# Performance work log

Hardware: AMD Instinct MI355X
Metric: run time of the kernel (lower is better)

The kernel has to match this reference:

```python
import jax, jax.numpy as jnp
import numpy as np

B, T, D, H, E, K = 2, 1024, 1024, 16, 8, 2
HS = D // H
FF = 4 * D


def layernorm(x, g, b, eps=1e-5):
    m = jnp.mean(x, axis=-1, keepdims=True)
    v = jnp.mean((x - m) ** 2, axis=-1, keepdims=True)
    return (x - m) * jax.lax.rsqrt(v + eps) * g + b


def setup_inputs() -> dict:
    key = jax.random.key(0)
    ks = jax.random.split(key, 10)
    s = 0.02
    return {
        "x": jax.random.normal(ks[0], (B, T, D), jnp.float32),
        "Wq": jax.random.normal(ks[1], (H, D, HS), jnp.float32) * s,
        "Wk": jax.random.normal(ks[2], (H, D, HS), jnp.float32) * s,
        "Wv": jax.random.normal(ks[3], (H, D, HS), jnp.float32) * s,
        "gate_W": jax.random.normal(ks[4], (D, E), jnp.float32) * s,
        "W1": jax.random.normal(ks[5], (E, D, FF), jnp.float32) * s,
        "b1": jnp.zeros((E, FF), jnp.float32),
        "W2": jax.random.normal(ks[6], (E, FF, D), jnp.float32) * s,
        "b2": jnp.zeros((E, D), jnp.float32),
        "ln1_g": jnp.ones((D,), jnp.float32),
        "ln1_b": jnp.zeros((D,), jnp.float32),
        "ln2_g": jnp.ones((D,), jnp.float32),
        "ln2_b": jnp.zeros((D,), jnp.float32),
    }


def reference(x, Wq, Wk, Wv, gate_W, W1, b1, W2, b2, ln1_g, ln1_b, ln2_g, ln2_b):
    b, t, d = x.shape
    # --- multi-head causal attention (note: original scales by n_embed**-0.5) ---
    q = jnp.einsum("btd,hdf->bhtf", x, Wq)
    k = jnp.einsum("btd,hdf->bhtf", x, Wk)
    v = jnp.einsum("btd,hdf->bhtf", x, Wv)
    wei = jnp.einsum("bhtf,bhsf->bhts", q, k) * (d ** -0.5)
    mask = jnp.tril(jnp.ones((t, t), bool))
    wei = jnp.where(mask, wei, -jnp.inf)
    wei = jax.nn.softmax(wei, axis=-1)
    attn = jnp.einsum("bhts,bhsf->bhtf", wei, v)
    attn = attn.transpose(0, 2, 1, 3).reshape(b, t, d)  # concat heads

    y = x + layernorm(attn, ln1_g, ln1_b)

    # --- MoE: top-k gate, softmax over selected logits, weighted combine ---
    flat = y.reshape(-1, d)                         # [N, D]
    logits = flat @ gate_W                          # [N, E]
    topv, topi = jax.lax.top_k(logits, K)           # [N, K]
    w = jax.nn.softmax(topv, axis=-1)               # [N, K]
    combine = jnp.sum(jax.nn.one_hot(topi, E, dtype=flat.dtype) * w[..., None], axis=1)  # [N, E]

    h = jax.nn.relu(jnp.einsum("nd,edf->enf", flat, W1) + b1[:, None, :])  # [E, N, FF]
    eo = jnp.einsum("enf,efd->end", h, W2) + b2[:, None, :]                # [E, N, D]
    moe = jnp.einsum("ne,end->nd", combine, eo)                            # [N, D]

    out = y + layernorm(moe.reshape(b, t, d), ln2_g, ln2_b)
    return out
```

## Files before the change

### kernel.cpp

```cpp
#include <hip/hip_runtime.h>
#include <hip/hip_bf16.h>
#include <math.h>

typedef short short8 __attribute__((ext_vector_type(8)));
typedef float floatx4 __attribute__((ext_vector_type(4)));
typedef unsigned int u32_g __attribute__((address_space(1)));
typedef unsigned int u32_l __attribute__((address_space(3)));

__device__ __forceinline__ void gl_lds16(const void* g, void* l) {
    __builtin_amdgcn_global_load_lds((const u32_g*)g, (u32_l*)l, 16, 0, 0);
}

#define NB 2
#define TSEQ 1024
#define DIM 1024
#define NHEAD 16
#define HS 64
#define NEXP 8
#define FF 4096
#define NTOK (NB*TSEQ)
#define MAXSLOT 5120

#define OFF_Q      ((size_t)0)
#define OFF_K      ((size_t)8388608)
#define OFF_V      ((size_t)16777216)
#define OFF_ATTN   ((size_t)25165824)
#define OFF_Y      ((size_t)33554432)
#define OFF_YBF    ((size_t)41943040)
#define OFF_W1T    ((size_t)46137344)
#define OFF_MOE    ((size_t)113246208)
#define OFF_TOPKE  ((size_t)121634816)
#define OFF_TOPKW  ((size_t)121651200)
#define OFF_CNT    ((size_t)121667584)
#define OFF_PO     ((size_t)121667648)
#define OFF_CUR    ((size_t)121667712)
#define OFF_SLOTT  ((size_t)121667776)
#define OFF_SLOTW  ((size_t)121688256)
#define OFF_S      ((size_t)121708800)
#define OFF_XHI    (OFF_S)
#define OFF_XLO    (OFF_S + 4194304)
#define OFF_WTHI   (OFF_S + 8388608)
#define OFF_WTLO   (OFF_S + 14680064)
#define OFF_W2T    (OFF_S)
#define OFF_H      (OFF_S + 67108864)

__global__ __launch_bounds__(256) void xsplit_kernel(
    const float* __restrict__ x, __hip_bfloat16* __restrict__ xhi, __hip_bfloat16* __restrict__ xlo)
{
    int idx = (blockIdx.x * 256 + threadIdx.x) * 4;
    float4 v = *(const float4*)(x + idx);
    float vv[4] = {v.x, v.y, v.z, v.w};
    union { ushort u[4]; ushort4 q; } hi, lo;
    #pragma unroll
    for (int l = 0; l < 4; ++l) {
        __hip_bfloat16 hb = __float2bfloat16(vv[l]);
        hi.u[l] = *(const ushort*)&hb;
        float r = vv[l] - __bfloat162float(hb);
        __hip_bfloat16 lb = __float2bfloat16(r);
        lo.u[l] = *(const ushort*)&lb;
    }
    *(ushort4*)((ushort*)xhi + idx) = hi.q;
    *(ushort4*)((ushort*)xlo + idx) = lo.q;
}

__global__ __launch_bounds__(256) void wsplit_kernel(
    const float* __restrict__ Wq, const float* __restrict__ Wk, const float* __restrict__ Wv,
    __hip_bfloat16* __restrict__ Wthi, __hip_bfloat16* __restrict__ Wtlo)
{
    int z = blockIdx.z, mat = z >> 4, hh = z & 15;
    const float* W = (mat == 0) ? Wq : ((mat == 1) ? Wk : Wv);
    const float* slab = W + (size_t)hh * DIM * HS;
    ushort* ohi = (ushort*)Wthi + (size_t)mat * (DIM * DIM) + (size_t)hh * HS * DIM;
    ushort* olo = (ushort*)Wtlo + (size_t)mat * (DIM * DIM) + (size_t)hh * HS * DIM;
    int c0 = blockIdx.x * 32, r0 = blockIdx.y * 32;
    __shared__ float tile[32][33];
    int t = threadIdx.x, i = t >> 3, j4 = (t & 7) * 4;
    float4 v4 = *(const float4*)(slab + (size_t)(r0 + i) * HS + c0 + j4);
    tile[i][j4] = v4.x; tile[i][j4+1] = v4.y; tile[i][j4+2] = v4.z; tile[i][j4+3] = v4.w;
    __syncthreads();
    union { ushort u[4]; ushort4 q; } hi, lo;
    #pragma unroll
    for (int l = 0; l < 4; ++l) {
        float xv = tile[j4 + l][i];
        __hip_bfloat16 hb = __float2bfloat16(xv);
        hi.u[l] = *(const ushort*)&hb;
        float r = xv - __bfloat162float(hb);
        __hip_bfloat16 lb = __float2bfloat16(r);
        lo.u[l] = *(const ushort*)&lb;
    }
    *(ushort4*)(ohi + (size_t)(c0 + i) * DIM + r0 + j4) = hi.q;
    *(ushort4*)(olo + (size_t)(c0 + i) * DIM + r0 + j4) = lo.q;
}

__global__ __launch_bounds__(256) void qkv_mfma(
    const __hip_bfloat16* __restrict__ xhi, const __hip_bfloat16* __restrict__ xlo,
    const __hip_bfloat16* __restrict__ Wthi, const __hip_bfloat16* __restrict__ Wtlo,
    float* __restrict__ Q, float* __restrict__ Kb, float* __restrict__ V)
{
    int mat = blockIdx.z;
    const __hip_bfloat16* Bhg = Wthi + (size_t)mat * (DIM * DIM);
    const __hip_bfloat16* Blg = Wtlo + (size_t)mat * (DIM * DIM);
    float* O = (mat == 0) ? Q : ((mat == 1) ? Kb : V);
    int n0 = blockIdx.x * 64, m0 = blockIdx.y * 128;
    int t = threadIdx.x, wave = t >> 6, lane = t & 63;
    __shared__ __hip_bfloat16 Ah[128][32];
    __shared__ __hip_bfloat16 Al[128][32];
    __shared__ __hip_bfloat16 Bh[64][32];
    __shared__ __hip_bfloat16 Bl[64][32];
    const __hip_bfloat16 *gAh[2], *gAl[2];
    __hip_bfloat16 *lAh[2], *lAl[2];
    #pragma unroll
    for (int p = 0; p < 2; ++p) {
        int lin = p * 256 + t, row = lin >> 2, seg = lin & 3;
        gAh[p] = xhi + (size_t)(m0 + row) * DIM + seg * 8;
        gAl[p] = xlo + (size_t)(m0 + row) * DIM + seg * 8;
        int cb = p * 256 + wave * 64;
        lAh[p] = &Ah[0][0] + (size_t)cb * 8;
        lAl[p] = &Al[0][0] + (size_t)cb * 8;
    }
    const __hip_bfloat16* gBh = Bhg + (size_t)(n0 + (t >> 2)) * DIM + (t & 3) * 8;
    const __hip_bfloat16* gBl = Blg + (size_t)(n0 + (t >> 2)) * DIM + (t & 3) * 8;
    __hip_bfloat16* lBh = &Bh[0][0] + (size_t)(wave * 64) * 8;
    __hip_bfloat16* lBl = &Bl[0][0] + (size_t)(wave * 64) * 8;

    int wr = (wave >> 1) * 64, wcl = (wave & 1) * 32;
    int lrow = lane & 15, quad = lane >> 4;
    floatx4 acc[4][2];
    #pragma unroll
    for (int i = 0; i < 4; ++i)
        #pragma unroll
        for (int j = 0; j < 2; ++j) acc[i][j] = (floatx4){0.f, 0.f, 0.f, 0.f};

    for (int k0 = 0; k0 < DIM; k0 += 32) {
        __syncthreads();
        gl_lds16(gAh[0] + k0, lAh[0]); gl_lds16(gAh[1] + k0, lAh[1]);
        gl_lds16(gAl[0] + k0, lAl[0]); gl_lds16(gAl[1] + k0, lAl[1]);
        gl_lds16(gBh + k0, lBh);       gl_lds16(gBl + k0, lBl);
        __syncthreads();
        short8 ah[4], al[4], bh[2], bl[2];
        #pragma unroll
        for (int i = 0; i < 4; ++i) {
            ah[i] = *(const short8*)(&Ah[wr + i * 16 + lrow][quad * 8]);
            al[i] = *(const short8*)(&Al[wr + i * 16 + lrow][quad * 8]);
        }
        #pragma unroll
        for (int j = 0; j < 2; ++j) {
            bh[j] = *(const short8*)(&Bh[wcl + j * 16 + lrow][quad * 8]);
            bl[j] = *(const short8*)(&Bl[wcl + j * 16 + lrow][quad * 8]);
        }
        #pragma unroll
        for (int i = 0; i < 4; ++i)
            #pragma unroll
            for (int j = 0; j < 2; ++j) {
                acc[i][j] = __builtin_amdgcn_mfma_f32_16x16x32_bf16(ah[i], bh[j], acc[i][j], 0, 0, 0);
                acc[i][j] = __builtin_amdgcn_mfma_f32_16x16x32_bf16(ah[i], bl[j], acc[i][j], 0, 0, 0);
                acc[i][j] = __builtin_amdgcn_mfma_f32_16x16x32_bf16(al[i], bh[j], acc[i][j], 0, 0, 0);
            }
    }
    #pragma unroll
    for (int i = 0; i < 4; ++i)
        #pragma unroll
        for (int j = 0; j < 2; ++j) {
            int ng = n0 + wcl + j * 16 + lrow;
            int hh = ng >> 6, f = ng & 63;
            #pragma unroll
            for (int r = 0; r < 4; ++r) {
                int mg = m0 + wr + i * 16 + quad * 4 + r;
                int bb = mg >> 10, tt = mg & 1023;
                O[(((size_t)bb * NHEAD + hh) * TSEQ + tt) * HS + f] = acc[i][j][r];
            }
        }
}

__global__ __launch_bounds__(256) void scores_kernel(
    const float* __restrict__ Q, const float* __restrict__ Kb, float* __restrict__ S)
{
    int tri = blockIdx.x, bh = blockIdx.y;
    int mt = 0; while (((mt + 1) * (mt + 2)) / 2 <= tri) ++mt;
    int nt = tri - (mt * (mt + 1)) / 2;
    int m0 = mt * 128, n0 = nt * 128;
    const float* Qb = Q + (size_t)bh * TSEQ * HS;
    const float* Kh = Kb + (size_t)bh * TSEQ * HS;
    float* Sb = S + (size_t)bh * TSEQ * TSEQ;
    __shared__ float As[16][132];
    __shared__ float Bs[16][132];
    int t = threadIdx.x, tx = t & 15, ty = t >> 4;
    float acc[8][8] = {{0.f}};
    for (int k0 = 0; k0 < HS; k0 += 16) {
        #pragma unroll
        for (int pss = 0; pss < 2; ++pss) {
            int lin = pss * 256 + t, m = lin >> 2, c = lin & 3;
            float4 v4 = *(const float4*)(Qb + (size_t)(m0 + m) * HS + k0 + c * 4);
            As[c*4+0][m] = v4.x; As[c*4+1][m] = v4.y; As[c*4+2][m] = v4.z; As[c*4+3][m] = v4.w;
        }
        #pragma unroll
        for (int pss = 0; pss < 2; ++pss) {
            int lin = pss * 256 + t, s = lin >> 2, c = lin & 3;
            float4 v4 = *(const float4*)(Kh + (size_t)(n0 + s) * HS + k0 + c * 4);
            Bs[c*4+0][s] = v4.x; Bs[c*4+1][s] = v4.y; Bs[c*4+2][s] = v4.z; Bs[c*4+3][s] = v4.w;
        }
        __syncthreads();
        #pragma unroll
        for (int kk = 0; kk < 16; ++kk) {
            float a[8], b[8];
            *(float4*)a       = *(const float4*)(&As[kk][ty * 4]);
            *(float4*)(a + 4) = *(const float4*)(&As[kk][64 + ty * 4]);
            *(float4*)b       = *(const float4*)(&Bs[kk][tx * 4]);
            *(float4*)(b + 4) = *(const float4*)(&Bs[kk][64 + tx * 4]);
            #pragma unroll
            for (int i = 0; i < 8; ++i)
                #pragma unroll
                for (int j = 0; j < 8; ++j) acc[i][j] += a[i] * b[j];
        }
        __syncthreads();
    }
    const float scale = 0.03125f;
    #pragma unroll
    for (int i = 0; i < 8; ++i) {
        int r = m0 + ((i < 4) ? ty * 4 + i : 64 + ty * 4 + (i - 4));
        #pragma unroll
        for (int jg = 0; jg < 2; ++jg) {
            int cb = n0 + ((jg == 0) ? tx * 4 : 64 + tx * 4);
            float4 v4 = make_float4(acc[i][jg*4+0]*scale, acc[i][jg*4+1]*scale,
                                    acc[i][jg*4+2]*scale, acc[i][jg*4+3]*scale);
            *(float4*)(Sb + (size_t)r * TSEQ + cb) = v4;
        }
    }
}

__global__ __launch_bounds__(256) void softmax_kernel(float* __restrict__ S)
{
    int row = blockIdx.x, bh = row >> 10, r = row & 1023;
    float* p = S + ((size_t)bh * TSEQ + r) * TSEQ;
    int len = r + 1, t = threadIdx.x;
    float v[4]; float mx = -1e30f;
    #pragma unroll
    for (int i = 0; i < 4; ++i) { int c = t + i * 256; v[i] = (c < len) ? p[c] : -1e30f; mx = fmaxf(mx, v[i]); }
    __shared__ float redA[4];
    #pragma unroll
    for (int off = 32; off; off >>= 1) mx = fmaxf(mx, __shfl_down(mx, off));
    if ((t & 63) == 0) redA[t >> 6] = mx;
    __syncthreads();
    mx = fmaxf(fmaxf(redA[0], redA[1]), fmaxf(redA[2], redA[3]));
    float sum = 0.f;
    #pragma unroll
    for (int i = 0; i < 4; ++i) { int c = t + i * 256; float e = (c < len) ? expf(v[i] - mx) : 0.f; v[i] = e; sum += e; }
    __shared__ float redB[4];
    #pragma unroll
    for (int off = 32; off; off >>= 1) sum += __shfl_down(sum, off);
    if ((t & 63) == 0) redB[t >> 6] = sum;
    __syncthreads();
    float inv = 1.f / (redB[0] + redB[1] + redB[2] + redB[3]);
    #pragma unroll
    for (int i = 0; i < 4; ++i) { int c = t + i * 256; p[c] = v[i] * inv; }
}

__global__ __launch_bounds__(256) void pv_kernel(
    const float* __restrict__ S, const float* __restrict__ V, float* __restrict__ attn)
{
    int mt = blockIdx.x, bh = blockIdx.y;
    int m0 = mt * 128;
    const float* P = S + (size_t)bh * TSEQ * TSEQ;
    const float* Vb = V + (size_t)bh * TSEQ * HS;
    __shared__ float As[16][132];
    __shared__ float Bs[16][68];
    int t = threadIdx.x, tx = t & 15, ty = t >> 4;
    float acc[8][4] = {{0.f}};
    int kend = m0 + 128;
    for (int k0 = 0; k0 < kend; k0 += 16) {
        #pragma unroll
        for (int pss = 0; pss < 2; ++pss) {
            int lin = pss * 256 + t, m = lin >> 2, c = lin & 3;
            float4 v4 = *(const float4*)(P + (size_t)(m0 + m) * TSEQ + k0 + c * 4);
            As[c*4+0][m] = v4.x; As[c*4+1][m] = v4.y; As[c*4+2][m] = v4.z; As[c*4+3][m] = v4.w;
        }
        { int kk = t >> 4, c = t & 15;
          float4 v4 = *(const float4*)(Vb + (size_t)(k0 + kk) * HS + c * 4);
          *(float4*)(&Bs[kk][c * 4]) = v4; }
        __syncthreads();
        #pragma unroll
        for (int kk = 0; kk < 16; ++kk) {
            float a[8], b[4];
            *(float4*)a       = *(const float4*)(&As[kk][ty * 4]);
            *(float4*)(a + 4) = *(const float4*)(&As[kk][64 + ty * 4]);
            *(float4*)b       = *(const float4*)(&Bs[kk][tx * 4]);
            #pragma unroll
            for (int i = 0; i < 8; ++i)
                #pragma unroll
                for (int j = 0; j < 4; ++j) acc[i][j] += a[i] * b[j];
        }
        __syncthreads();
    }
    int b = bh >> 4, hh = bh & 15;
    #pragma unroll
    for (int i = 0; i < 8; ++i) {
        int r = m0 + ((i < 4) ? ty * 4 + i : 64 + ty * 4 + (i - 4));
        float4 v4 = make_float4(acc[i][0], acc[i][1], acc[i][2], acc[i][3]);
        *(float4*)(attn + ((size_t)b * TSEQ + r) * DIM + hh * HS + tx * 4) = v4;
    }
}

__global__ __launch_bounds__(256) void ln1_kernel(
    const float* __restrict__ x, const float* __restrict__ attn,
    const float* __restrict__ g, const float* __restrict__ bta,
    float* __restrict__ y, __hip_bfloat16* __restrict__ ybf)
{
    int n = blockIdx.x, t = threadIdx.x;
    const float* a = attn + (size_t)n * DIM;
    float v[4]; float s = 0.f;
    #pragma unroll
    for (int i = 0; i < 4; ++i) { v[i] = a[t + i * 256]; s += v[i]; }
    __shared__ float redA[4];
    #pragma unroll
    for (int off = 32; off; off >>= 1) s += __shfl_down(s, off);
    if ((t & 63) == 0) redA[t >> 6] = s;
    __syncthreads();
    float mean = (redA[0] + redA[1] + redA[2] + redA[3]) * (1.f / 1024.f);
    float s2 = 0.f;
    #pragma unroll
    for (int i = 0; i < 4; ++i) { float d = v[i] - mean; s2 += d * d; }
    __shared__ float redB[4];
    #pragma unroll
    for (int off = 32; off; off >>= 1) s2 += __shfl_down(s2, off);
    if ((t & 63) == 0) redB[t >> 6] = s2;
    __syncthreads();
    float rstd = rsqrtf((redB[0] + redB[1] + redB[2] + redB[3]) * (1.f / 1024.f) + 1e-5f);
    #pragma unroll
    for (int i = 0; i < 4; ++i) {
        int d = t + i * 256;
        float val = x[(size_t)n * DIM + d] + (v[i] - mean) * rstd * g[d] + bta[d];
        y[(size_t)n * DIM + d] = val;
        ybf[(size_t)n * DIM + d] = __float2bfloat16(val);
    }
}

__global__ __launch_bounds__(256) void transpose_kernel(
    const float* __restrict__ in, __hip_bfloat16* __restrict__ out, int R, int C)
{
    const float* ie = in + (size_t)blockIdx.z * R * C;
    __hip_bfloat16* oe = out + (size_t)blockIdx.z * R * C;
    int c0 = blockIdx.x * 32, r0 = blockIdx.y * 32;
    __shared__ float tile[32][33];
    int t = threadIdx.x, i = t >> 3, j4 = (t & 7) * 4;
    float4 v4 = *(const float4*)(ie + (size_t)(r0 + i) * C + c0 + j4);
    tile[i][j4] = v4.x; tile[i][j4+1] = v4.y; tile[i][j4+2] = v4.z; tile[i][j4+3] = v4.w;
    __syncthreads();
    union { ushort u[4]; ushort4 v; } pk;
    #pragma unroll
    for (int l = 0; l < 4; ++l) {
        __hip_bfloat16 hb = __float2bfloat16(tile[j4 + l][i]);
        pk.u[l] = *(const ushort*)&hb;
    }
    *(ushort4*)((ushort*)oe + (size_t)(c0 + i) * R + r0 + j4) = pk.v;
}

__global__ __launch_bounds__(256) void gate_kernel(
    const float* __restrict__ y, const float* __restrict__ gW,
    int* __restrict__ topk_e, float* __restrict__ topk_w, int* __restrict__ cnt)
{
    int n = blockIdx.x, t = threadIdx.x;
    const float* yr = y + (size_t)n * DIM;
    float p[8] = {0.f,0.f,0.f,0.f,0.f,0.f,0.f,0.f};
    for (int d = t; d < DIM; d += 256) {
        float yv = yr[d];
        const float* w = gW + (size_t)d * NEXP;
        #pragma unroll
        for (int e = 0; e < 8; ++e) p[e] += yv * w[e];
    }
    #pragma unroll
    for (int e = 0; e < 8; ++e)
        #pragma unroll
        for (int off = 32; off; off >>= 1) p[e] += __shfl_down(p[e], off);
    __shared__ float lg[4][8];
    if ((t & 63) == 0) { int w = t >> 6;
        #pragma unroll
        for (int e = 0; e < 8; ++e) lg[w][e] = p[e]; }
    __syncthreads();
    if (t == 0) {
        float l[8];
        #pragma unroll
        for (int e = 0; e < 8; ++e) l[e] = lg[0][e] + lg[1][e] + lg[2][e] + lg[3][e];
        int e0 = 0; float v0 = l[0];
        for (int e = 1; e < 8; ++e) if (l[e] > v0) { v0 = l[e]; e0 = e; }
        int e1 = 0; float v1 = -1e30f;
        for (int e = 0; e < 8; ++e) if (e != e0 && l[e] > v1) { v1 = l[e]; e1 = e; }
        float z = expf(v1 - v0);
        float w0 = 1.f / (1.f + z), w1 = z / (1.f + z);
        topk_e[n * 2] = e0; topk_e[n * 2 + 1] = e1;
        topk_w[n * 2] = w0; topk_w[n * 2 + 1] = w1;
        atomicAdd(&cnt[e0], 1); atomicAdd(&cnt[e1], 1);
    }
}

__global__ void scan_kernel(const int* __restrict__ cnt, int* __restrict__ po, int* __restrict__ cursor)
{
    if (threadIdx.x == 0 && blockIdx.x == 0) {
        int acc = 0;
        for (int e = 0; e < 8; ++e) { po[e] = acc; cursor[e] = acc; acc += ((cnt[e] + 127) >> 7) << 7; }
        po[8] = acc;
    }
}

__global__ void scatter_kernel(const int* __restrict__ topk_e, const float* __restrict__ topk_w,
                               int* __restrict__ cursor, int* __restrict__ slot_token, float* __restrict__ slot_w)
{
    int i = blockIdx.x * 256 + threadIdx.x;
    int e = topk_e[i];
    int pos = atomicAdd(&cursor[e], 1);
    slot_token[pos] = i >> 1;
    slot_w[pos] = topk_w[i];
}

__global__ __launch_bounds__(256) void moe_gemm1(
    const __hip_bfloat16* __restrict__ ybf, const __hip_bfloat16* __restrict__ W1t,
    const float* __restrict__ b1, const int* __restrict__ po, const int* __restrict__ cnt,
    const int* __restrict__ slot_token, __hip_bfloat16* __restrict__ h)
{
    int m0 = blockIdx.y * 128;
    int total = po[8];
    if (m0 >= total) return;
    int e = 0;
    for (int i = 0; i < 8; ++i) if (m0 >= po[i] && m0 < po[i + 1]) e = i;
    int valid = po[e] + cnt[e] - m0; if (valid > 128) valid = 128;
    int n0 = blockIdx.x * 128;
    int t = threadIdx.x, wave = t >> 6, lane = t & 63;
    __shared__ int tok[128];
    __shared__ __hip_bfloat16 As[128][64];
    __shared__ __hip_bfloat16 Bs[128][64];
    if (t < 128) tok[t] = (t < valid) ? slot_token[m0 + t] : slot_token[m0];
    __syncthreads();
    const __hip_bfloat16 *gA[4], *gB[4];
    __hip_bfloat16 *lA[4], *lB[4];
    #pragma unroll
    for (int p = 0; p < 4; ++p) {
        int lin = p * 256 + t, row = lin >> 3, seg = lin & 7;
        gA[p] = ybf + (size_t)tok[row] * DIM + seg * 8;
        gB[p] = W1t + ((size_t)e * FF + n0 + row) * DIM + seg * 8;
        int cb = p * 256 + wave * 64;
        lA[p] = &As[0][0] + (size_t)cb * 8;
        lB[p] = &Bs[0][0] + (size_t)cb * 8;
    }
    int wr = (wave >> 1) * 64, wc = (wave & 1) * 64;
    int lrow = lane & 15, quad = lane >> 4;
    floatx4 acc[4][4];
    #pragma unroll
    for (int i = 0; i < 4; ++i)
        #pragma unroll
        for (int j = 0; j < 4; ++j) acc[i][j] = (floatx4){0.f, 0.f, 0.f, 0.f};
    for (int k0 = 0; k0 < DIM; k0 += 64) {
        __syncthreads();
        #pragma unroll
        for (int p = 0; p < 4; ++p) { gl_lds16(gA[p] + k0, lA[p]); gl_lds16(gB[p] + k0, lB[p]); }
        __syncthreads();
        #pragma unroll
        for (int ks = 0; ks < 2; ++ks) {
            short8 a[4], b[4];
            #pragma unroll
            for (int i = 0; i < 4; ++i) a[i] = *(const short8*)(&As[wr + i * 16 + lrow][ks * 32 + quad * 8]);
            #pragma unroll
            for (int j = 0; j < 4; ++j) b[j] = *(const short8*)(&Bs[wc + j * 16 + lrow][ks * 32 + quad * 8]);
            #pragma unroll
            for (int i = 0; i < 4; ++i)
                #pragma unroll
                for (int j = 0; j < 4; ++j)
                    acc[i][j] = __builtin_amdgcn_mfma_f32_16x16x32_bf16(a[i], b[j], acc[i][j], 0, 0, 0);
        }
    }
    #pragma unroll
    for (int i = 0; i < 4; ++i)
        #pragma unroll
        for (int j = 0; j < 4; ++j) {
            int col = n0 + wc + j * 16 + lrow;
            float bias = b1[e * FF + col];
            #pragma unroll
            for (int r = 0; r < 4; ++r) {
                int row = wr + i * 16 + quad * 4 + r;
                float vv = fmaxf(acc[i][j][r] + bias, 0.f);
                h[(size_t)(m0 + row) * FF + col] = __float2bfloat16(vv);
            }
        }
}

__global__ __launch_bounds__(256) void moe_gemm2(
    const __hip_bfloat16* __restrict__ h, const __hip_bfloat16* __restrict__ W2t,
    const float* __restrict__ b2, const int* __restrict__ po, const int* __restrict__ cnt,
    const int* __restrict__ slot_token, const float* __restrict__ slot_w, float* __restrict__ moe)
{
    int m0 = blockIdx.y * 128;
    int total = po[8];
    if (m0 >= total) return;
    int e = 0;
    for (int i = 0; i < 8; ++i) if (m0 >= po[i] && m0 < po[i + 1]) e = i;
    int valid = po[e] + cnt[e] - m0; if (valid > 128) valid = 128;
    int n0 = blockIdx.x * 128;
    int kz = blockIdx.z;
    int t = threadIdx.x, wave = t >> 6, lane = t & 63;
    __shared__ int tokS[128];
    __shared__ float wS[128];
    __shared__ __hip_bfloat16 As[128][64];
    __shared__ __hip_bfloat16 Bs[128][64];
    if (t < 128) {
        tokS[t] = (t < valid) ? slot_token[m0 + t] : 0;
        wS[t]   = (t < valid) ? slot_w[m0 + t] : 0.f;
    }
    __syncthreads();
    const __hip_bfloat16 *gA[4], *gB[4];
    __hip_bfloat16 *lA[4], *lB[4];
    #pragma unroll
    for (int p = 0; p < 4; ++p) {
        int lin = p * 256 + t, row = lin >> 3, seg = lin & 7;
        gA[p] = h + (size_t)(m0 + row) * FF + seg * 8;
        gB[p] = W2t + ((size_t)e * DIM + n0 + row) * FF + seg * 8;
        int cb = p * 256 + wave * 64;
        lA[p] = &As[0][0] + (size_t)cb * 8;
        lB[p] = &Bs[0][0] + (size_t)cb * 8;
    }
    int wr = (wave >> 1) * 64, wc = (wave & 1) * 64;
    int lrow = lane & 15, quad = lane >> 4;
    floatx4 acc[4][4];
    #pragma unroll
    for (int i = 0; i < 4; ++i)
        #pragma unroll
        for (int j = 0; j < 4; ++j) acc[i][j] = (floatx4){0.f, 0.f, 0.f, 0.f};
    int kbeg = kz * (FF / 2), kend = kbeg + (FF / 2);
    for (int k0 = kbeg; k0 < kend; k0 += 64) {
        __syncthreads();
        #pragma unroll
        for (int p = 0; p < 4; ++p) { gl_lds16(gA[p] + k0, lA[p]); gl_lds16(gB[p] + k0, lB[p]); }
        __syncthreads();
        #pragma unroll
        for (int ks = 0; ks < 2; ++ks) {
            short8 a[4], b[4];
            #pragma unroll
            for (int i = 0; i < 4; ++i) a[i] = *(const short8*)(&As[wr + i * 16 + lrow][ks * 32 + quad * 8]);
            #pragma unroll
            for (int j = 0; j < 4; ++j) b[j] = *(const short8*)(&Bs[wc + j * 16 + lrow][ks * 32 + quad * 8]);
            #pragma unroll
            for (int i = 0; i < 4; ++i)
                #pragma unroll
                for (int j = 0; j < 4; ++j)
                    acc[i][j] = __builtin_amdgcn_mfma_f32_16x16x32_bf16(a[i], b[j], acc[i][j], 0, 0, 0);
        }
    }
    #pragma unroll
    for (int i = 0; i < 4; ++i)
        #pragma unroll
        for (int j = 0; j < 4; ++j) {
            int col = n0 + wc + j * 16 + lrow;
            float bias = (kz == 0) ? b2[e * DIM + col] : 0.f;
            #pragma unroll
            for (int r = 0; r < 4; ++r) {
                int row = wr + i * 16 + quad * 4 + r;
                if (row < valid) {
                    float vv = acc[i][j][r] + bias;
                    atomicAdd(&moe[(size_t)tokS[row] * DIM + col], wS[row] * vv);
                }
            }
        }
}

__global__ __launch_bounds__(256) void ln2_kernel(
    const float* __restrict__ y, const float* __restrict__ moe,
    const float* __restrict__ g, const float* __restrict__ bta, float* __restrict__ out)
{
    int n = blockIdx.x, t = threadIdx.x;
    const float* a = moe + (size_t)n * DIM;
    float v[4]; float s = 0.f;
    #pragma unroll
    for (int i = 0; i < 4; ++i) { v[i] = a[t + i * 256]; s += v[i]; }
    __shared__ float redA[4];
    #pragma unroll
    for (int off = 32; off; off >>= 1) s += __shfl_down(s, off);
    if ((t & 63) == 0) redA[t >> 6] = s;
    __syncthreads();
    float mean = (redA[0] + redA[1] + redA[2] + redA[3]) * (1.f / 1024.f);
    float s2 = 0.f;
    #pragma unroll
    for (int i = 0; i < 4; ++i) { float d = v[i] - mean; s2 += d * d; }
    __shared__ float redB[4];
    #pragma unroll
    for (int off = 32; off; off >>= 1) s2 += __shfl_down(s2, off);
    if ((t & 63) == 0) redB[t >> 6] = s2;
    __syncthreads();
    float rstd = rsqrtf((redB[0] + redB[1] + redB[2] + redB[3]) * (1.f / 1024.f) + 1e-5f);
    #pragma unroll
    for (int i = 0; i < 4; ++i) {
        int d = t + i * 256;
        out[(size_t)n * DIM + d] = y[(size_t)n * DIM + d] + (v[i] - mean) * rstd * g[d] + bta[d];
    }
}

extern "C" void kernel_launch(void* const* d_in, const int* in_sizes, int n_in,
                              void* d_out, int out_size, void* d_ws, size_t ws_size,
                              hipStream_t stream)
{
    const float* x    = (const float*)d_in[0];
    const float* Wq   = (const float*)d_in[1];
    const float* Wk   = (const float*)d_in[2];
    const float* Wv   = (const float*)d_in[3];
    const float* gW   = (const float*)d_in[4];
    const float* W1   = (const float*)d_in[5];
    const float* b1   = (const float*)d_in[6];
    const float* W2   = (const float*)d_in[7];
    const float* b2   = (const float*)d_in[8];
    const float* ln1g = (const float*)d_in[9];
    const float* ln1b = (const float*)d_in[10];
    const float* ln2g = (const float*)d_in[11];
    const float* ln2b = (const float*)d_in[12];
    float* out = (float*)d_out;

    char* ws = (char*)d_ws;
    float* Q    = (float*)(ws + OFF_Q);
    float* Kb   = (float*)(ws + OFF_K);
    float* V    = (float*)(ws + OFF_V);
    float* attn = (float*)(ws + OFF_ATTN);
    float* y    = (float*)(ws + OFF_Y);
    __hip_bfloat16* ybf = (__hip_bfloat16*)(ws + OFF_YBF);
    __hip_bfloat16* W1t = (__hip_bfloat16*)(ws + OFF_W1T);
    float* moe  = (float*)(ws + OFF_MOE);
    int*   topk_e = (int*)(ws + OFF_TOPKE);
    float* topk_w = (float*)(ws + OFF_TOPKW);
    int*   cnt    = (int*)(ws + OFF_CNT);
    int*   po     = (int*)(ws + OFF_PO);
    int*   cur    = (int*)(ws + OFF_CUR);
    int*   slot_t = (int*)(ws + OFF_SLOTT);
    float* slot_w = (float*)(ws + OFF_SLOTW);
    float* S      = (float*)(ws + OFF_S);
    __hip_bfloat16* xhi  = (__hip_bfloat16*)(ws + OFF_XHI);
    __hip_bfloat16* xlo  = (__hip_bfloat16*)(ws + OFF_XLO);
    __hip_bfloat16* Wthi = (__hip_bfloat16*)(ws + OFF_WTHI);
    __hip_bfloat16* Wtlo = (__hip_bfloat16*)(ws + OFF_WTLO);
    __hip_bfloat16* W2t = (__hip_bfloat16*)(ws + OFF_W2T);
    __hip_bfloat16* h   = (__hip_bfloat16*)(ws + OFF_H);

    hipMemsetAsync(cnt, 0, 32, stream);
    hipMemsetAsync(moe, 0, (size_t)NTOK * DIM * 4, stream);

    xsplit_kernel<<<2048, 256, 0, stream>>>(x, xhi, xlo);
    wsplit_kernel<<<dim3(2, 32, 48), 256, 0, stream>>>(Wq, Wk, Wv, Wthi, Wtlo);
    qkv_mfma<<<dim3(16, 16, 3), 256, 0, stream>>>(xhi, xlo, Wthi, Wtlo, Q, Kb, V);
    scores_kernel<<<dim3(36, 32), 256, 0, stream>>>(Q, Kb, S);
    softmax_kernel<<<NB * NHEAD * TSEQ, 256, 0, stream>>>(S);
    pv_kernel<<<dim3(8, 32), 256, 0, stream>>>(S, V, attn);
    ln1_kernel<<<NTOK, 256, 0, stream>>>(x, attn, ln1g, ln1b, y, ybf);
    transpose_kernel<<<dim3(128, 32, 8), 256, 0, stream>>>(W1, W1t, DIM, FF);
    transpose_kernel<<<dim3(32, 128, 8), 256, 0, stream>>>(W2, W2t, FF, DIM);
    gate_kernel<<<NTOK, 256, 0, stream>>>(y, gW, topk_e, topk_w, cnt);
    scan_kernel<<<1, 64, 0, stream>>>(cnt, po, cur);
    scatter_kernel<<<16, 256, 0, stream>>>(topk_e, topk_w, cur, slot_t, slot_w);
    moe_gemm1<<<dim3(32, 40), 256, 0, stream>>>(ybf, W1t, b1, po, cnt, slot_t, h);
    moe_gemm2<<<dim3(8, 40, 2), 256, 0, stream>>>(h, W2t, b2, po, cnt, slot_t, slot_w, moe);
    ln2_kernel<<<NTOK, 256, 0, stream>>>(y, moe, ln2g, ln2b, out);
}
```

Measured before the change: 855.3 us.

## Split PV over K halves, trim softmax stores, remap MoE grids for XCD locality

The PV kernel now splits the causal key range into two halves across blockIdx.z. Each half writes its own partial output buffer, and LN1 sums the two, which doubles PV parallelism and evens out per-block work. Softmax stops writing zeros beyond the 128-aligned causal limit, cutting store traffic. The MoE GEMMs use flat 1D grids that assign the same N-tile to the same XCD for L2 reuse, and each weight transpose is moved to sit just before the GEMM that uses it. Risks: attnB aliases the Q buffer (OFF_Q), which works only because Q is dead after scores, and there is an extra partial-buffer read in LN1.

```diff
diff --git a/kernel.cpp b/kernel.cpp
--- a/kernel.cpp
+++ b/kernel.cpp
@@ -44,6 +44,8 @@
 #define OFF_W2T    (OFF_S)
 #define OFF_H      (OFF_S + 67108864)
 
+#define OFF_ATTNB  (OFF_Q)
+
 __global__ __launch_bounds__(256) void xsplit_kernel(
     const float* __restrict__ x, __hip_bfloat16* __restrict__ xhi, __hip_bfloat16* __restrict__ xlo)
 {
@@ -233,6 +235,7 @@
     int row = blockIdx.x, bh = row >> 10, r = row & 1023;
     float* p = S + ((size_t)bh * TSEQ + r) * TSEQ;
     int len = r + 1, t = threadIdx.x;
+    int klim = (r & ~127) + 128;
     float v[4]; float mx = -1e30f;
     #pragma unroll
     for (int i = 0; i < 4; ++i) { int c = t + i * 256; v[i] = (c < len) ? p[c] : -1e30f; mx = fmaxf(mx, v[i]); }
@@ -252,22 +255,26 @@
     __syncthreads();
     float inv = 1.f / (redB[0] + redB[1] + redB[2] + redB[3]);
     #pragma unroll
-    for (int i = 0; i < 4; ++i) { int c = t + i * 256; p[c] = v[i] * inv; }
+    for (int i = 0; i < 4; ++i) { int c = t + i * 256; if (c < klim) p[c] = v[i] * inv; }
 }
 
 __global__ __launch_bounds__(256) void pv_kernel(
-    const float* __restrict__ S, const float* __restrict__ V, float* __restrict__ attn)
-{
-    int mt = blockIdx.x, bh = blockIdx.y;
+    const float* __restrict__ S, const float* __restrict__ V,
+    float* __restrict__ attn, float* __restrict__ attnB)
+{
+    int mt = blockIdx.x, bh = blockIdx.y, z = blockIdx.z;
     int m0 = mt * 128;
+    int half = (m0 >> 1) + 64;
+    int kbeg = z ? half : 0;
+    int kend = z ? (m0 + 128) : half;
+    float* O = z ? attnB : attn;
     const float* P = S + (size_t)bh * TSEQ * TSEQ;
     const float* Vb = V + (size_t)bh * TSEQ * HS;
     __shared__ float As[16][132];
     __shared__ float Bs[16][68];
     int t = threadIdx.x, tx = t & 15, ty = t >> 4;
     float acc[8][4] = {{0.f}};
-    int kend = m0 + 128;
-    for (int k0 = 0; k0 < kend; k0 += 16) {
+    for (int k0 = kbeg; k0 < kend; k0 += 16) {
         #pragma unroll
         for (int pss = 0; pss < 2; ++pss) {
             int lin = pss * 256 + t, m = lin >> 2, c = lin & 3;
@@ -296,20 +303,21 @@
     for (int i = 0; i < 8; ++i) {
         int r = m0 + ((i < 4) ? ty * 4 + i : 64 + ty * 4 + (i - 4));
         float4 v4 = make_float4(acc[i][0], acc[i][1], acc[i][2], acc[i][3]);
-        *(float4*)(attn + ((size_t)b * TSEQ + r) * DIM + hh * HS + tx * 4) = v4;
+        *(float4*)(O + ((size_t)b * TSEQ + r) * DIM + hh * HS + tx * 4) = v4;
     }
 }
 
 __global__ __launch_bounds__(256) void ln1_kernel(
-    const float* __restrict__ x, const float* __restrict__ attn,
+    const float* __restrict__ x, const float* __restrict__ attn, const float* __restrict__ attnB,
     const float* __restrict__ g, const float* __restrict__ bta,
     float* __restrict__ y, __hip_bfloat16* __restrict__ ybf)
 {
     int n = blockIdx.x, t = threadIdx.x;
     const float* a = attn + (size_t)n * DIM;
+    const float* aB = attnB + (size_t)n * DIM;
     float v[4]; float s = 0.f;
     #pragma unroll
-    for (int i = 0; i < 4; ++i) { v[i] = a[t + i * 256]; s += v[i]; }
+    for (int i = 0; i < 4; ++i) { int c = t + i * 256; v[i] = a[c] + aB[c]; s += v[i]; }
     __shared__ float redA[4];
     #pragma unroll
     for (int off = 32; off; off >>= 1) s += __shfl_down(s, off);
@@ -416,13 +424,15 @@
     const float* __restrict__ b1, const int* __restrict__ po, const int* __restrict__ cnt,
     const int* __restrict__ slot_token, __hip_bfloat16* __restrict__ h)
 {
-    int m0 = blockIdx.y * 128;
+    int flat = blockIdx.x;
+    int xcd = flat & 7, j = flat >> 3;
+    int n0 = (((j & 3) << 3) + xcd) * 128;
+    int m0 = (j >> 2) * 128;
     int total = po[8];
     if (m0 >= total) return;
     int e = 0;
     for (int i = 0; i < 8; ++i) if (m0 >= po[i] && m0 < po[i + 1]) e = i;
     int valid = po[e] + cnt[e] - m0; if (valid > 128) valid = 128;
-    int n0 = blockIdx.x * 128;
     int t = threadIdx.x, wave = t >> 6, lane = t & 63;
     __shared__ int tok[128];
     __shared__ __hip_bfloat16 As[128][64];
@@ -446,7 +456,7 @@
     #pragma unroll
     for (int i = 0; i < 4; ++i)
         #pragma unroll
-        for (int j = 0; j < 4; ++j) acc[i][j] = (floatx4){0.f, 0.f, 0.f, 0.f};
+        for (int j2 = 0; j2 < 4; ++j2) acc[i][j2] = (floatx4){0.f, 0.f, 0.f, 0.f};
     for (int k0 = 0; k0 < DIM; k0 += 64) {
         __syncthreads();
         #pragma unroll
@@ -458,24 +468,24 @@
             #pragma unroll
             for (int i = 0; i < 4; ++i) a[i] = *(const short8*)(&As[wr + i * 16 + lrow][ks * 32 + quad * 8]);
             #pragma unroll
-            for (int j = 0; j < 4; ++j) b[j] = *(const short8*)(&Bs[wc + j * 16 + lrow][ks * 32 + quad * 8]);
+            for (int j2 = 0; j2 < 4; ++j2) b[j2] = *(const short8*)(&Bs[wc + j2 * 16 + lrow][ks * 32 + quad * 8]);
             #pragma unroll
             for (int i = 0; i < 4; ++i)
                 #pragma unroll
-                for (int j = 0; j < 4; ++j)
-                    acc[i][j] = __builtin_amdgcn_mfma_f32_16x16x32_bf16(a[i], b[j], acc[i][j], 0, 0, 0);
+                for (int j2 = 0; j2 < 4; ++j2)
+                    acc[i][j2] = __builtin_amdgcn_mfma_f32_16x16x32_bf16(a[i], b[j2], acc[i][j2], 0, 0, 0);
         }
     }
     #pragma unroll
     for (int i = 0; i < 4; ++i)
         #pragma unroll
-        for (int j = 0; j < 4; ++j) {
-            int col = n0 + wc + j * 16 + lrow;
+        for (int j2 = 0; j2 < 4; ++j2) {
+            int col = n0 + wc + j2 * 16 + lrow;
             float bias = b1[e * FF + col];
             #pragma unroll
             for (int r = 0; r < 4; ++r) {
                 int row = wr + i * 16 + quad * 4 + r;
-                float vv = fmaxf(acc[i][j][r] + bias, 0.f);
+                float vv = fmaxf(acc[i][j2][r] + bias, 0.f);
                 h[(size_t)(m0 + row) * FF + col] = __float2bfloat16(vv);
             }
         }
@@ -486,14 +496,16 @@
     const float* __restrict__ b2, const int* __restrict__ po, const int* __restrict__ cnt,
     const int* __restrict__ slot_token, const float* __restrict__ slot_w, float* __restrict__ moe)
 {
-    int m0 = blockIdx.y * 128;
+    int flat = blockIdx.x;
+    int xcd = flat & 7, j = flat >> 3;
+    int n0 = xcd * 128;
+    int kz = j & 1;
+    int m0 = (j >> 1) * 128;
     int total = po[8];
     if (m0 >= total) return;
     int e = 0;
     for (int i = 0; i < 8; ++i) if (m0 >= po[i] && m0 < po[i + 1]) e = i;
     int valid = po[e] + cnt[e] - m0; if (valid > 128) valid = 128;
-    int n0 = blockIdx.x * 128;
-    int kz = blockIdx.z;
     int t = threadIdx.x, wave = t >> 6, lane = t & 63;
     __shared__ int tokS[128];
     __shared__ float wS[128];
@@ -521,7 +533,7 @@
     #pragma unroll
     for (int i = 0; i < 4; ++i)
         #pragma unroll
-        for (int j = 0; j < 4; ++j) acc[i][j] = (floatx4){0.f, 0.f, 0.f, 0.f};
+        for (int j2 = 0; j2 < 4; ++j2) acc[i][j2] = (floatx4){0.f, 0.f, 0.f, 0.f};
     int kbeg = kz * (FF / 2), kend = kbeg + (FF / 2);
     for (int k0 = kbeg; k0 < kend; k0 += 64) {
         __syncthreads();
@@ -534,25 +546,25 @@
             #pragma unroll
             for (int i = 0; i < 4; ++i) a[i] = *(const short8*)(&As[wr + i * 16 + lrow][ks * 32 + quad * 8]);
             #pragma unroll
-            for (int j = 0; j < 4; ++j) b[j] = *(const short8*)(&Bs[wc + j * 16 + lrow][ks * 32 + quad * 8]);
+            for (int j2 = 0; j2 < 4; ++j2) b[j2] = *(const short8*)(&Bs[wc + j2 * 16 + lrow][ks * 32 + quad * 8]);
             #pragma unroll
             for (int i = 0; i < 4; ++i)
                 #pragma unroll
-                for (int j = 0; j < 4; ++j)
-                    acc[i][j] = __builtin_amdgcn_mfma_f32_16x16x32_bf16(a[i], b[j], acc[i][j], 0, 0, 0);
+                for (int j2 = 0; j2 < 4; ++j2)
+                    acc[i][j2] = __builtin_amdgcn_mfma_f32_16x16x32_bf16(a[i], b[j2], acc[i][j2], 0, 0, 0);
         }
     }
     #pragma unroll
     for (int i = 0; i < 4; ++i)
         #pragma unroll
-        for (int j = 0; j < 4; ++j) {
-            int col = n0 + wc + j * 16 + lrow;
+        for (int j2 = 0; j2 < 4; ++j2) {
+            int col = n0 + wc + j2 * 16 + lrow;
             float bias = (kz == 0) ? b2[e * DIM + col] : 0.f;
             #pragma unroll
             for (int r = 0; r < 4; ++r) {
                 int row = wr + i * 16 + quad * 4 + r;
                 if (row < valid) {
-                    float vv = acc[i][j][r] + bias;
+                    float vv = acc[i][j2][r] + bias;
                     atomicAdd(&moe[(size_t)tokS[row] * DIM + col], wS[row] * vv);
                 }
             }
@@ -614,6 +626,7 @@
     float* Kb   = (float*)(ws + OFF_K);
     float* V    = (float*)(ws + OFF_V);
     float* attn = (float*)(ws + OFF_ATTN);
+    float* attnB= (float*)(ws + OFF_ATTNB);
     float* y    = (float*)(ws + OFF_Y);
     __hip_bfloat16* ybf = (__hip_bfloat16*)(ws + OFF_YBF);
     __hip_bfloat16* W1t = (__hip_bfloat16*)(ws + OFF_W1T);
@@ -641,14 +654,14 @@
     qkv_mfma<<<dim3(16, 16, 3), 256, 0, stream>>>(xhi, xlo, Wthi, Wtlo, Q, Kb, V);
     scores_kernel<<<dim3(36, 32), 256, 0, stream>>>(Q, Kb, S);
     softmax_kernel<<<NB * NHEAD * TSEQ, 256, 0, stream>>>(S);
-    pv_kernel<<<dim3(8, 32), 256, 0, stream>>>(S, V, attn);
-    ln1_kernel<<<NTOK, 256, 0, stream>>>(x, attn, ln1g, ln1b, y, ybf);
-    transpose_kernel<<<dim3(128, 32, 8), 256, 0, stream>>>(W1, W1t, DIM, FF);
-    transpose_kernel<<<dim3(32, 128, 8), 256, 0, stream>>>(W2, W2t, FF, DIM);
+    pv_kernel<<<dim3(8, 32, 2), 256, 0, stream>>>(S, V, attn, attnB);
+    ln1_kernel<<<NTOK, 256, 0, stream>>>(x, attn, attnB, ln1g, ln1b, y, ybf);
     gate_kernel<<<NTOK, 256, 0, stream>>>(y, gW, topk_e, topk_w, cnt);
     scan_kernel<<<1, 64, 0, stream>>>(cnt, po, cur);
     scatter_kernel<<<16, 256, 0, stream>>>(topk_e, topk_w, cur, slot_t, slot_w);
-    moe_gemm1<<<dim3(32, 40), 256, 0, stream>>>(ybf, W1t, b1, po, cnt, slot_t, h);
-    moe_gemm2<<<dim3(8, 40, 2), 256, 0, stream>>>(h, W2t, b2, po, cnt, slot_t, slot_w, moe);
+    transpose_kernel<<<dim3(128, 32, 8), 256, 0, stream>>>(W1, W1t, DIM, FF);
+    moe_gemm1<<<1280, 256, 0, stream>>>(ybf, W1t, b1, po, cnt, slot_t, h);
+    transpose_kernel<<<dim3(32, 128, 8), 256, 0, stream>>>(W2, W2t, FF, DIM);
+    moe_gemm2<<<640, 256, 0, stream>>>(h, W2t, b2, po, cnt, slot_t, slot_w, moe);
     ln2_kernel<<<NTOK, 256, 0, stream>>>(y, moe, ln2g, ln2b, out);
 }
```

New measurement: 836.3 us. -2.2%, faster.
